# Kernel optimization log

Hardware: AMD Instinct MI355X
Metric: run time of the kernel (lower is better)

The kernel has to match this reference:

```python
import jax, jax.numpy as jnp
import numpy as np

K = 7  # local_kernel_size


def conv2d(x, w, b, pad):
    # x: [B,C,H,W], w: [O,I,kh,kw]
    y = jax.lax.conv_general_dilated(
        x, w, window_strides=(1, 1), padding=[(pad, pad), (pad, pad)],
        dimension_numbers=("NCHW", "OIHW", "NCHW"))
    return y + b[None, :, None, None]


def kernel_normalize(kernel, k):
    # kernel: [B, k*k, H, W]; zero-mean over tap dim, then add 1/(k*k)
    km = jnp.mean(kernel, axis=1, keepdims=True)
    return kernel - km + 1.0 / (k * k)


def local_conv_feat(img, kernel, k):
    # Fused dynamic local conv: avoids materializing [B,C,k*k,H,W].
    # Tap order matches F.unfold row-major (dy, dx).
    B, C, H, W = img.shape
    pad = (k - 1) // 2
    imgp = jnp.pad(img, ((0, 0), (0, 0), (pad, pad), (pad, pad)))
    out = jnp.zeros_like(img)
    for dy in range(k):
        for dx in range(k):
            idx = dy * k + dx
            out = out + imgp[:, :, dy:dy + H, dx:dx + W] * kernel[:, idx:idx + 1]
    return out


def setup_inputs() -> dict:
    key = jax.random.key(0)
    ks = jax.random.split(key, 14)
    B, C, H, W = 4, 64, 128, 128
    w = lambda k, shape: jax.random.normal(k, shape, jnp.float32) * 0.05
    return {
        "x": jax.random.normal(ks[0], (B, C, H, W), jnp.float32),
        "kernel_features": jax.random.normal(ks[1], (B, C, H, W), jnp.float32),
        # feature_path: two 3x3 convs
        "fw1": w(ks[2], (C, C, 3, 3)), "fb1": jnp.zeros((C,), jnp.float32),
        "fw2": w(ks[3], (C, C, 3, 3)), "fb2": jnp.zeros((C,), jnp.float32),
        # multiplicative_path: two 3x3 convs
        "mw1": w(ks[4], (C, C, 3, 3)), "mb1": jnp.zeros((C,), jnp.float32),
        "mw2": w(ks[5], (C, C, 3, 3)), "mb2": jnp.zeros((C,), jnp.float32),
        # local_filter_path: two 1x1 convs, last outputs k*k channels
        "lw1": w(ks[6], (C, C, 1, 1)), "lb1": jnp.zeros((C,), jnp.float32),
        "lw2": w(ks[7], (K * K, C, 1, 1)), "lb2": jnp.zeros((K * K,), jnp.float32),
    }


def reference(x, kernel_features, fw1, fb1, fw2, fb2, mw1, mb1, mw2, mb2, lw1, lb1, lw2, lb2):
    # feature_path: ReLU -> conv3x3 -> ReLU -> conv3x3
    fp = conv2d(jax.nn.relu(conv2d(jax.nn.relu(x), fw1, fb1, 1)), fw2, fb2, 1)
    # multiplicative_path: conv3x3 -> ReLU -> conv3x3
    mp = conv2d(jax.nn.relu(conv2d(kernel_features, mw1, mb1, 1)), mw2, mb2, 1)
    # local_filter_path: conv1x1 -> ReLU -> conv1x1 (-> k*k channels)
    lp = conv2d(jax.nn.relu(conv2d(kernel_features, lw1, lb1, 0)), lw2, lb2, 0)
    lp = kernel_normalize(lp, K)
    feat = fp * mp
    filtered = local_conv_feat(feat, lp, K)
    return x + filtered
```

## Files before the change

kernel.cpp:

```cpp
#include <hip/hip_runtime.h>
#include <hip/hip_bf16.h>

#define Cc 64
#define Hc 128
#define Wc 128
#define HWc (Hc * Wc)
#define Bc 4

typedef __attribute__((ext_vector_type(8))) short short8;
typedef __attribute__((ext_vector_type(4))) float float4v;

static __device__ __forceinline__ unsigned short f2bu(float f) {
    __hip_bfloat16 h = __float2bfloat16(f);
    return *(unsigned short*)&h;
}
static __device__ __forceinline__ float bulo(unsigned int u) {
    return __uint_as_float((u & 0xffffu) << 16);
}
static __device__ __forceinline__ float buhi(unsigned int u) {
    return __uint_as_float(u & 0xffff0000u);
}

static __device__ __forceinline__ void gl_lds16(const void* g, void* l) {
    __builtin_amdgcn_global_load_lds(
        (const __attribute__((address_space(1))) unsigned int*)g,
        (__attribute__((address_space(3))) unsigned int*)l, 16, 0, 0);
}

__global__ __launch_bounds__(256) void prep_k(
    const float* __restrict__ x, const float* __restrict__ kf,
    const float* __restrict__ fw1, const float* __restrict__ fw2,
    const float* __restrict__ mw1, const float* __restrict__ mw2,
    const float* __restrict__ lw1, const float* __restrict__ lw2,
    unsigned short* __restrict__ xb, unsigned short* __restrict__ kfb,
    unsigned short* __restrict__ wbase, unsigned short* __restrict__ zpage)
{
    const int bid = blockIdx.x;
    const int tid = threadIdx.x;

    if (bid < 512) {
        const bool isx = bid < 256;
        const float* src = isx ? x : kf;
        unsigned short* dst = isx ? xb : kfb;
        const int px = (isx ? bid : bid - 256) * 256 + tid;
        const int b  = px >> 14;
        const int hw = px & 16383;
        const float* s = src + (size_t)b * Cc * HWc + hw;
        unsigned short* d = dst + (size_t)px * Cc;
#pragma unroll
        for (int c8 = 0; c8 < 8; ++c8) {
            unsigned int pk[4];
#pragma unroll
            for (int jp = 0; jp < 4; ++jp) {
                float v0 = s[(size_t)(c8 * 8 + jp * 2 + 0) * HWc];
                float v1 = s[(size_t)(c8 * 8 + jp * 2 + 1) * HWc];
                if (isx) { v0 = fmaxf(v0, 0.f); v1 = fmaxf(v1, 0.f); }
                pk[jp] = (unsigned int)f2bu(v0) | ((unsigned int)f2bu(v1) << 16);
            }
            *(uint4*)(d + c8 * 8) = make_uint4(pk[0], pk[1], pk[2], pk[3]);
        }
    } else if (bid < 584) {
        const int wbid  = bid - 512;
        const int which = wbid / 18;
        const float* w = (which == 0) ? fw1 : (which == 1) ? fw2 : (which == 2) ? mw1 : mw2;
        unsigned short* wb = wbase + (size_t)which * 36864;
        const int g = (wbid % 18) * 256 + tid;
        if (g >= 4608) return;
        const int lane = g & 63;
        const int smt  = g >> 6;
        const int s    = smt >> 2;
        const int mt   = smt & 3;
        const int co   = mt * 16 + (lane & 15);
        const int kb   = s * 32 + (lane >> 4) * 8;
        unsigned int pk[4];
#pragma unroll
        for (int jp = 0; jp < 4; ++jp) {
            int k0 = kb + jp * 2, k1 = k0 + 1;
            float v0 = w[((size_t)co * Cc + (k0 & 63)) * 9 + (k0 >> 6)];
            float v1 = w[((size_t)co * Cc + (k1 & 63)) * 9 + (k1 >> 6)];
            pk[jp] = (unsigned int)f2bu(v0) | ((unsigned int)f2bu(v1) << 16);
        }
        *(uint4*)(wb + (size_t)g * 8) = make_uint4(pk[0], pk[1], pk[2], pk[3]);
    } else if (bid < 588) {
        const int wbid  = bid - 584;
        const int which = wbid >> 1;
        const float* w = which ? lw2 : lw1;
        const int Cout = which ? 49 : 64;
        unsigned short* wb = wbase + 4 * 36864 + (size_t)which * 4096;
        const int g = (wbid & 1) * 256 + tid;
        const int lane = g & 63;
        const int smt  = g >> 6;
        const int s    = smt >> 2;
        const int mt   = smt & 3;
        const int co   = mt * 16 + (lane & 15);
        const int kb   = s * 32 + (lane >> 4) * 8;
        unsigned int pk[4];
#pragma unroll
        for (int jp = 0; jp < 4; ++jp) {
            int k0 = kb + jp * 2, k1 = k0 + 1;
            float v0 = (co < Cout) ? w[(size_t)co * Cc + k0] : 0.f;
            float v1 = (co < Cout) ? w[(size_t)co * Cc + k1] : 0.f;
            pk[jp] = (unsigned int)f2bu(v0) | ((unsigned int)f2bu(v1) << 16);
        }
        *(uint4*)(wb + (size_t)g * 8) = make_uint4(pk[0], pk[1], pk[2], pk[3]);
    } else {
        if (tid < 64) ((unsigned int*)zpage)[tid] = 0;
    }
}

#define STAGE_DMA(INPTR, SBUF)                                                \
    for (int k = wv; k < 33; k += 4) {                                        \
        const int u_  = k * 8 + (lane >> 3);                                  \
        const int j_  = lane & 7;                                             \
        const int r_  = u_ / 66;                                              \
        const int c_  = u_ - r_ * 66;                                         \
        const int gh_ = h0 - 1 + r_;                                          \
        const int gw_ = w0 - 1 + c_;                                          \
        const bool ok_ = ((unsigned)gh_ < (unsigned)Hc) && ((unsigned)gw_ < (unsigned)Wc); \
        const int ch_ = j_ ^ (u_ & 7);                                        \
        const unsigned short* g_ = ok_                                        \
            ? (INPTR) + ((((size_t)b * Hc + gh_) * Wc + gw_) << 6) + (ch_ << 3) \
            : zpage + (ch_ << 3);                                             \
        gl_lds16(g_, &(SBUF)[k * 512]);                                       \
    }

#define LOAD_A(W, s, m) (*(const short8*)((W) + (size_t)(s) * 2048 + (size_t)(m) * 512))
#define LOAD_B(SB, s, nt) ({                                                  \
        const int tap_ = (s) >> 1;                                            \
        const int qb_  = rowb[tap_ / 3] + tap_ % 3;                           \
        const int ch0_ = ((s) & 1) * 4 + quad;                                \
        *(const short8*)&(SB)[(qb_ + (nt) * 16) * 64 + ((ch0_ ^ (qb_ & 7)) << 3)]; })

#define CONV_GEMM(APTR, ACC, SB)                                              \
    {                                                                         \
        short8 a_buf[4][2], b_cur[4], b_nxt[4];                               \
        _Pragma("unroll")                                                     \
        for (int q = 0; q < 3; ++q)                                           \
            _Pragma("unroll")                                                 \
            for (int m = 0; m < 2; ++m) a_buf[q][m] = LOAD_A(APTR, q, m);     \
        _Pragma("unroll")                                                     \
        for (int nt = 0; nt < 4; ++nt) b_cur[nt] = LOAD_B(SB, 0, nt);         \
        _Pragma("unroll")                                                     \
        for (int s = 0; s < 18; ++s) {                                        \
            if (s + 3 < 18) {                                                 \
                _Pragma("unroll")                                             \
                for (int m = 0; m < 2; ++m)                                   \
                    a_buf[(s + 3) & 3][m] = LOAD_A(APTR, s + 3, m);           \
            }                                                                 \
            if (s + 1 < 18) {                                                 \
                _Pragma("unroll")                                             \
                for (int nt = 0; nt < 4; ++nt)                                \
                    b_nxt[nt] = LOAD_B(SB, s + 1, nt);                        \
            }                                                                 \
            _Pragma("unroll")                                                 \
            for (int nt = 0; nt < 4; ++nt)                                    \
                _Pragma("unroll")                                             \
                for (int m = 0; m < 2; ++m)                                   \
                    ACC[m][nt] = __builtin_amdgcn_mfma_f32_16x16x32_bf16(     \
                        a_buf[s & 3][m], b_cur[nt], ACC[m][nt], 0, 0, 0);     \
            if (s + 1 < 18) {                                                 \
                _Pragma("unroll")                                             \
                for (int nt = 0; nt < 4; ++nt) b_cur[nt] = b_nxt[nt];         \
            }                                                                 \
        }                                                                     \
    }

__global__ __launch_bounds__(256) void conv1_lp_k(
    const unsigned short* __restrict__ in0,
    const unsigned short* __restrict__ in1,
    const unsigned short* __restrict__ wfrag0,
    const unsigned short* __restrict__ wfrag1,
    const float* __restrict__ bias0,
    const float* __restrict__ bias1,
    const unsigned short* __restrict__ zpage,
    unsigned short* __restrict__ out0,
    unsigned short* __restrict__ out1,
    const unsigned short* __restrict__ w1, const float* __restrict__ b1,
    const unsigned short* __restrict__ w2, const float* __restrict__ b2,
    unsigned short* __restrict__ lpout)
{
    __shared__ unsigned short s_b[264 * 64];

    const int tid  = threadIdx.x;
    const int lane = tid & 63;
    const int wv   = tid >> 6;
    const int quad = lane >> 4;
    const int glin = blockIdx.x;
    const int xcd  = glin & 7;
    const int slot = glin >> 3;

    if (slot < 128) {
        const int sel = slot >> 6;
        const int hti = slot & 63;
        const int b   = xcd >> 1;
        const int w0  = (xcd & 1) * 64;
        const int h0  = hti * 2;

        const unsigned short* in    = sel ? in1 : in0;
        const unsigned short* wfrag = sel ? wfrag1 : wfrag0;
        const float*          bias  = sel ? bias1 : bias0;
        unsigned short*       out   = sel ? out1 : out0;

        STAGE_DMA(in, s_b);
        __syncthreads();

        const int rowsel = wv >> 1;
        const int cohalf = wv & 1;
        const int n15    = lane & 15;
        const unsigned short* aptr = wfrag + (((size_t)(cohalf * 2) * 64 + lane) << 3);

        int rowb[3];
#pragma unroll
        for (int ky = 0; ky < 3; ++ky) rowb[ky] = (rowsel + ky) * 66 + n15;

        float4v acc[2][4];
#pragma unroll
        for (int m = 0; m < 2; ++m)
#pragma unroll
            for (int nt = 0; nt < 4; ++nt) acc[m][nt] = (float4v){0.f, 0.f, 0.f, 0.f};

        CONV_GEMM(aptr, acc, s_b);

        const int h = h0 + rowsel;
#pragma unroll
        for (int m = 0; m < 2; ++m) {
            const int mt  = cohalf * 2 + m;
            const int co0 = mt * 16 + quad * 4;
            float4 bv = *(const float4*)&bias[co0];
#pragma unroll
            for (int nt = 0; nt < 4; ++nt) {
                const size_t pix = ((size_t)b * Hc + h) * Wc + w0 + nt * 16 + n15;
                ushort4 pk;
                pk.x = f2bu(fmaxf(acc[m][nt][0] + bv.x, 0.f));
                pk.y = f2bu(fmaxf(acc[m][nt][1] + bv.y, 0.f));
                pk.z = f2bu(fmaxf(acc[m][nt][2] + bv.z, 0.f));
                pk.w = f2bu(fmaxf(acc[m][nt][3] + bv.w, 0.f));
                *(ushort4*)&out[pix * Cc + co0] = pk;
            }
        }
    } else {
        const int lpid = xcd * 128 + (slot - 128);
        const int p    = lane & 15;
        const size_t pix = (size_t)lpid * 64 + wv * 16 + p;
        unsigned short* st = &s_b[wv * 1024];

        float4v acc1[4];
#pragma unroll
        for (int mt = 0; mt < 4; ++mt) acc1[mt] = (float4v){0.f, 0.f, 0.f, 0.f};
#pragma unroll
        for (int s = 0; s < 2; ++s) {
            short8 bfr = *(const short8*)&in1[pix * Cc + s * 32 + quad * 8];
#pragma unroll
            for (int mt = 0; mt < 4; ++mt) {
                short8 afr = *(const short8*)&w1[(size_t)(((s * 4 + mt) << 6) + lane) << 3];
                acc1[mt] = __builtin_amdgcn_mfma_f32_16x16x32_bf16(afr, bfr, acc1[mt], 0, 0, 0);
            }
        }

#pragma unroll
        for (int mt = 0; mt < 4; ++mt) {
            const int co0 = mt * 16 + quad * 4;
            float4 bv = *(const float4*)&b1[co0];
            ushort4 pk;
            pk.x = f2bu(fmaxf(acc1[mt][0] + bv.x, 0.f));
            pk.y = f2bu(fmaxf(acc1[mt][1] + bv.y, 0.f));
            pk.z = f2bu(fmaxf(acc1[mt][2] + bv.z, 0.f));
            pk.w = f2bu(fmaxf(acc1[mt][3] + bv.w, 0.f));
            const int cg = co0 >> 3;
            *(ushort4*)&st[p * 64 + ((cg ^ (p & 7)) << 3) + (quad & 1) * 4] = pk;
        }
        __syncthreads();

        float4v acc2[4];
#pragma unroll
        for (int mt = 0; mt < 4; ++mt) acc2[mt] = (float4v){0.f, 0.f, 0.f, 0.f};
#pragma unroll
        for (int s = 0; s < 2; ++s) {
            const int cg = s * 4 + quad;
            short8 bfr = *(const short8*)&st[p * 64 + ((cg ^ (p & 7)) << 3)];
#pragma unroll
            for (int mt = 0; mt < 4; ++mt) {
                short8 afr = *(const short8*)&w2[(size_t)(((s * 4 + mt) << 6) + lane) << 3];
                acc2[mt] = __builtin_amdgcn_mfma_f32_16x16x32_bf16(afr, bfr, acc2[mt], 0, 0, 0);
            }
        }

        float v[4][4];
        float partial = 0.f;
#pragma unroll
        for (int mt = 0; mt < 4; ++mt) {
#pragma unroll
            for (int r = 0; r < 4; ++r) {
                const int tap = mt * 16 + quad * 4 + r;
                float val = (tap < 49) ? (acc2[mt][r] + b2[tap]) : 0.f;
                v[mt][r] = val;
                partial += val;
            }
        }
        partial += __shfl_xor(partial, 16, 64);
        partial += __shfl_xor(partial, 32, 64);
        const float m = partial * (1.f / 49.f) - (1.f / 49.f);

        const int b  = (int)(pix >> 14);
        const int hw = (int)(pix & 16383);
#pragma unroll
        for (int mt = 0; mt < 4; ++mt) {
#pragma unroll
            for (int r = 0; r < 4; ++r) {
                const int tap = mt * 16 + quad * 4 + r;
                if (tap < 49)
                    lpout[((size_t)b * 49 + tap) * HWc + hw] = f2bu(v[mt][r] - m);
            }
        }
    }
}

__global__ __launch_bounds__(256) void conv2_fused_k(
    const unsigned short* __restrict__ t1f,
    const unsigned short* __restrict__ t1m,
    const unsigned short* __restrict__ wf,
    const unsigned short* __restrict__ wm,
    const float* __restrict__ bf,
    const float* __restrict__ bm,
    const unsigned short* __restrict__ zpage,
    unsigned short* __restrict__ featp)
{
    __shared__ unsigned short s_b2[2][264 * 64];

    const int tid  = threadIdx.x;
    const int lane = tid & 63;
    const int wv   = tid >> 6;
    const int glin = blockIdx.x;
    const int xcd  = glin & 7;
    const int slot = glin >> 3;
    const int b    = xcd >> 1;
    const int w0   = (xcd & 1) * 64;
    const int h0   = slot * 2;

    STAGE_DMA(t1f, s_b2[0]);
    STAGE_DMA(t1m, s_b2[1]);
    __syncthreads();

    const int rowsel = wv >> 1;
    const int cohalf = wv & 1;
    const int quad   = lane >> 4;
    const int n15    = lane & 15;

    int rowb[3];
#pragma unroll
    for (int ky = 0; ky < 3; ++ky) rowb[ky] = (rowsel + ky) * 66 + n15;

    float4v acc[2][4];
#pragma unroll
    for (int m = 0; m < 2; ++m)
#pragma unroll
        for (int nt = 0; nt < 4; ++nt) acc[m][nt] = (float4v){0.f, 0.f, 0.f, 0.f};

    {
        const unsigned short* aptr = wf + (((size_t)(cohalf * 2) * 64 + lane) << 3);
        CONV_GEMM(aptr, acc, s_b2[0]);
    }

    float fpv[2][4][4];
#pragma unroll
    for (int m = 0; m < 2; ++m) {
        const int mt  = cohalf * 2 + m;
        const int co0 = mt * 16 + quad * 4;
        float4 bv = *(const float4*)&bf[co0];
#pragma unroll
        for (int nt = 0; nt < 4; ++nt) {
            fpv[m][nt][0] = bulo((unsigned int)f2bu(acc[m][nt][0] + bv.x));
            fpv[m][nt][1] = bulo((unsigned int)f2bu(acc[m][nt][1] + bv.y));
            fpv[m][nt][2] = bulo((unsigned int)f2bu(acc[m][nt][2] + bv.z));
            fpv[m][nt][3] = bulo((unsigned int)f2bu(acc[m][nt][3] + bv.w));
        }
    }

#pragma unroll
    for (int m = 0; m < 2; ++m)
#pragma unroll
        for (int nt = 0; nt < 4; ++nt) acc[m][nt] = (float4v){0.f, 0.f, 0.f, 0.f};

    {
        const unsigned short* aptr = wm + (((size_t)(cohalf * 2) * 64 + lane) << 3);
        CONV_GEMM(aptr, acc, s_b2[1]);
    }

    const int h = h0 + rowsel;
#pragma unroll
    for (int m = 0; m < 2; ++m) {
        const int mt  = cohalf * 2 + m;
        const int co0 = mt * 16 + quad * 4;
        float4 bv = *(const float4*)&bm[co0];
#pragma unroll
        for (int nt = 0; nt < 4; ++nt) {
            const int px = h * Wc + w0 + nt * 16 + n15;
            float v[4] = {acc[m][nt][0] + bv.x, acc[m][nt][1] + bv.y,
                          acc[m][nt][2] + bv.z, acc[m][nt][3] + bv.w};
#pragma unroll
            for (int r = 0; r < 4; ++r)
                featp[((size_t)b * Cc + co0 + r) * HWc + px] =
                    f2bu(v[r] * fpv[m][nt][r]);
        }
    }
}

__global__ __launch_bounds__(256) void local_conv_v4(
    const float* __restrict__ x, const unsigned short* __restrict__ featp,
    const unsigned short* __restrict__ lp, float* __restrict__ out)
{
    const int tid  = threadIdx.x;
    const int glin = blockIdx.x;
    const int xcd  = glin & 7;
    const int slot = glin >> 3;
    const int pair = xcd * 8 + (slot >> 4);
    const int cg   = slot & 15;
    const int b    = pair >> 4;
    const int hti  = pair & 15;

    const int w4  = (tid & 31) * 4;
    const int ro  = tid >> 5;
    const int h   = hti * 8 + ro;
    const int c0  = cg * 4;

    float msk[12];
#pragma unroll
    for (int e = 0; e < 12; ++e) {
        int gw = w4 - 4 + e;
        msk[e] = ((unsigned)gw < (unsigned)Wc) ? 1.f : 0.f;
    }

    float acc[4][4];
#pragma unroll
    for (int ch = 0; ch < 4; ++ch)
#pragma unroll
        for (int p = 0; p < 4; ++p) acc[ch][p] = 0.f;

    const unsigned short* lpb = lp + (size_t)b * 49 * HWc + (size_t)h * Wc + w4;
    const unsigned short* fb  = featp + ((size_t)b * Cc + c0) * HWc;

#pragma unroll
    for (int dy = 0; dy < 7; ++dy) {
        const int gh = h + dy - 3;
        if ((unsigned)gh >= (unsigned)Hc) continue;

        float lpf[7][4];
#pragma unroll
        for (int dx = 0; dx < 7; ++dx) {
            uint2 lv = *(const uint2*)&lpb[(size_t)(dy * 7 + dx) * HWc];
            lpf[dx][0] = bulo(lv.x); lpf[dx][1] = buhi(lv.x);
            lpf[dx][2] = bulo(lv.y); lpf[dx][3] = buhi(lv.y);
        }

        const unsigned short* frow = fb + (size_t)gh * Wc + w4;
#pragma unroll
        for (int ch = 0; ch < 4; ++ch) {
            const unsigned short* fr = frow + (size_t)ch * HWc;
            uint2 a  = *(const uint2*)(fr - 4);
            uint2 bq = *(const uint2*)(fr);
            uint2 cq = *(const uint2*)(fr + 4);
            float f[12];
            f[0]  = bulo(a.x);             f[1]  = buhi(a.x) * msk[1];
            f[2]  = bulo(a.y) * msk[2];    f[3]  = buhi(a.y) * msk[3];
            f[4]  = bulo(bq.x);            f[5]  = buhi(bq.x);
            f[6]  = bulo(bq.y);            f[7]  = buhi(bq.y);
            f[8]  = bulo(cq.x) * msk[8];   f[9]  = buhi(cq.x) * msk[9];
            f[10] = bulo(cq.y) * msk[10];  f[11] = buhi(cq.y);
#pragma unroll
            for (int dx = 0; dx < 7; ++dx)
#pragma unroll
                for (int p = 0; p < 4; ++p)
                    acc[ch][p] = fmaf(f[p + dx + 1], lpf[dx][p], acc[ch][p]);
        }
    }

#pragma unroll
    for (int ch = 0; ch < 4; ++ch) {
        const size_t idx = ((size_t)b * Cc + c0 + ch) * HWc + (size_t)h * Wc + w4;
        float4 xv = *(const float4*)&x[idx];
        float4 r  = {acc[ch][0] + xv.x, acc[ch][1] + xv.y,
                     acc[ch][2] + xv.z, acc[ch][3] + xv.w};
        *(float4*)&out[idx] = r;
    }
}

extern "C" void kernel_launch(void* const* d_in, const int* in_sizes, int n_in,
                              void* d_out, int out_size, void* d_ws, size_t ws_size,
                              hipStream_t stream)
{
    const float* x   = (const float*)d_in[0];
    const float* kf  = (const float*)d_in[1];
    const float* fw1 = (const float*)d_in[2];
    const float* fb1 = (const float*)d_in[3];
    const float* fw2 = (const float*)d_in[4];
    const float* fb2 = (const float*)d_in[5];
    const float* mw1 = (const float*)d_in[6];
    const float* mb1 = (const float*)d_in[7];
    const float* mw2 = (const float*)d_in[8];
    const float* mb2 = (const float*)d_in[9];
    const float* lw1 = (const float*)d_in[10];
    const float* lb1 = (const float*)d_in[11];
    const float* lw2 = (const float*)d_in[12];
    const float* lb2 = (const float*)d_in[13];

    float* out = (float*)d_out;
    char*  ws  = (char*)d_ws;

    const size_t NBH = (size_t)Bc * HWc * Cc * 2;
    const size_t LPH = (size_t)Bc * 49 * HWc * 2;
    const size_t WBA = (size_t)(4 * 36864 + 2 * 4096) * 2;

    unsigned short* t1f   = (unsigned short*)(ws);
    unsigned short* t1m   = (unsigned short*)(ws + NBH);
    unsigned short* featp = (unsigned short*)(ws + 2 * NBH);
    unsigned short* lpb   = (unsigned short*)(ws + 3 * NBH);
    unsigned short* xb    = (unsigned short*)(ws + 3 * NBH + LPH);
    unsigned short* kfb   = (unsigned short*)((char*)xb + NBH);
    unsigned short* wbase = (unsigned short*)((char*)kfb + NBH);
    unsigned short* zpage = (unsigned short*)((char*)wbase + WBA);
    unsigned short* wb1   = wbase;
    unsigned short* wb2   = wbase + 36864;
    unsigned short* wb3   = wbase + 2 * 36864;
    unsigned short* wb4   = wbase + 3 * 36864;
    unsigned short* wl1   = wbase + 4 * 36864;
    unsigned short* wl2   = wbase + 4 * 36864 + 4096;

    dim3 blk(256);

    prep_k<<<dim3(589), blk, 0, stream>>>(x, kf, fw1, fw2, mw1, mw2, lw1, lw2,
                                          xb, kfb, wbase, zpage);

    conv1_lp_k<<<dim3(2048), blk, 0, stream>>>(xb, kfb, wb1, wb3, fb1, mb1, zpage,
                                               t1f, t1m, wl1, lb1, wl2, lb2, lpb);

    conv2_fused_k<<<dim3(512), blk, 0, stream>>>(t1f, t1m, wb2, wb4, fb2, mb2,
                                                 zpage, featp);

    local_conv_v4<<<dim3(1024), blk, 0, stream>>>(x, featp, lpb, out);
}
```

Before: 161.6 us.

## Fuse local-filter 1x1 path into kf conv blocks and vectorize prep transpose

The separate local-filter-path blocks in conv1_lp_k are removed. Each block that convolves kernel_features now also computes the two 1x1 convs and the tap normalization for the pixels it just staged, which halves the grid. The prep kernel's NCHW to NHWC bf16 conversion now uses float4 loads, with each thread handling four pixels, so fewer blocks are needed. The zero page is also enlarged. The fusion adds imbalance, since only half the conv blocks carry the extra 1x1 work, and it lengthens the per-block critical path.

```diff
diff --git a/kernel.cpp b/kernel.cpp
--- a/kernel.cpp
+++ b/kernel.cpp
@@ -19,6 +19,9 @@
 }
 static __device__ __forceinline__ float buhi(unsigned int u) {
     return __uint_as_float(u & 0xffff0000u);
+}
+static __device__ __forceinline__ unsigned int pk2(float a, float b) {
+    return (unsigned int)f2bu(a) | ((unsigned int)f2bu(b) << 16);
 }
 
 static __device__ __forceinline__ void gl_lds16(const void* g, void* l) {
@@ -38,29 +41,40 @@
     const int bid = blockIdx.x;
     const int tid = threadIdx.x;
 
-    if (bid < 512) {
-        const bool isx = bid < 256;
-        const float* src = isx ? x : kf;
-        unsigned short* dst = isx ? xb : kfb;
-        const int px = (isx ? bid : bid - 256) * 256 + tid;
-        const int b  = px >> 14;
-        const int hw = px & 16383;
-        const float* s = src + (size_t)b * Cc * HWc + hw;
-        unsigned short* d = dst + (size_t)px * Cc;
-#pragma unroll
-        for (int c8 = 0; c8 < 8; ++c8) {
-            unsigned int pk[4];
+    if (bid < 256) {
+        const int gid    = bid * 256 + tid;
+        const int tensor = gid >> 15;
+        const int b      = (gid >> 13) & 3;
+        const int chalf  = (gid >> 12) & 1;
+        const int px     = (gid & 4095) * 4;
+        const bool isx   = (tensor == 0);
+        const float* s = (isx ? x : kf) + ((size_t)(b * Cc + chalf * 32)) * HWc + px;
+        unsigned short* d = (isx ? xb : kfb) + ((size_t)((size_t)b * HWc + px)) * Cc + chalf * 32;
+#pragma unroll
+        for (int c8 = 0; c8 < 4; ++c8) {
+            unsigned int pk[4][4];
 #pragma unroll
             for (int jp = 0; jp < 4; ++jp) {
-                float v0 = s[(size_t)(c8 * 8 + jp * 2 + 0) * HWc];
-                float v1 = s[(size_t)(c8 * 8 + jp * 2 + 1) * HWc];
-                if (isx) { v0 = fmaxf(v0, 0.f); v1 = fmaxf(v1, 0.f); }
-                pk[jp] = (unsigned int)f2bu(v0) | ((unsigned int)f2bu(v1) << 16);
+                float4 v0 = *(const float4*)(s + (size_t)(c8 * 8 + jp * 2 + 0) * HWc);
+                float4 v1 = *(const float4*)(s + (size_t)(c8 * 8 + jp * 2 + 1) * HWc);
+                if (isx) {
+                    v0.x = fmaxf(v0.x, 0.f); v0.y = fmaxf(v0.y, 0.f);
+                    v0.z = fmaxf(v0.z, 0.f); v0.w = fmaxf(v0.w, 0.f);
+                    v1.x = fmaxf(v1.x, 0.f); v1.y = fmaxf(v1.y, 0.f);
+                    v1.z = fmaxf(v1.z, 0.f); v1.w = fmaxf(v1.w, 0.f);
+                }
+                pk[0][jp] = pk2(v0.x, v1.x);
+                pk[1][jp] = pk2(v0.y, v1.y);
+                pk[2][jp] = pk2(v0.z, v1.z);
+                pk[3][jp] = pk2(v0.w, v1.w);
             }
-            *(uint4*)(d + c8 * 8) = make_uint4(pk[0], pk[1], pk[2], pk[3]);
-        }
-    } else if (bid < 584) {
-        const int wbid  = bid - 512;
+#pragma unroll
+            for (int i = 0; i < 4; ++i)
+                *(uint4*)(d + (size_t)i * Cc + c8 * 8) =
+                    make_uint4(pk[i][0], pk[i][1], pk[i][2], pk[i][3]);
+        }
+    } else if (bid < 328) {
+        const int wbid  = bid - 256;
         const int which = wbid / 18;
         const float* w = (which == 0) ? fw1 : (which == 1) ? fw2 : (which == 2) ? mw1 : mw2;
         unsigned short* wb = wbase + (size_t)which * 36864;
@@ -78,11 +92,11 @@
             int k0 = kb + jp * 2, k1 = k0 + 1;
             float v0 = w[((size_t)co * Cc + (k0 & 63)) * 9 + (k0 >> 6)];
             float v1 = w[((size_t)co * Cc + (k1 & 63)) * 9 + (k1 >> 6)];
-            pk[jp] = (unsigned int)f2bu(v0) | ((unsigned int)f2bu(v1) << 16);
+            pk[jp] = pk2(v0, v1);
         }
         *(uint4*)(wb + (size_t)g * 8) = make_uint4(pk[0], pk[1], pk[2], pk[3]);
-    } else if (bid < 588) {
-        const int wbid  = bid - 584;
+    } else if (bid < 332) {
+        const int wbid  = bid - 328;
         const int which = wbid >> 1;
         const float* w = which ? lw2 : lw1;
         const int Cout = which ? 49 : 64;
@@ -100,11 +114,13 @@
             int k0 = kb + jp * 2, k1 = k0 + 1;
             float v0 = (co < Cout) ? w[(size_t)co * Cc + k0] : 0.f;
             float v1 = (co < Cout) ? w[(size_t)co * Cc + k1] : 0.f;
-            pk[jp] = (unsigned int)f2bu(v0) | ((unsigned int)f2bu(v1) << 16);
+            pk[jp] = pk2(v0, v1);
         }
         *(uint4*)(wb + (size_t)g * 8) = make_uint4(pk[0], pk[1], pk[2], pk[3]);
     } else {
-        if (tid < 64) ((unsigned int*)zpage)[tid] = 0;
+        uint4 z = make_uint4(0u, 0u, 0u, 0u);
+        ((uint4*)zpage)[tid] = z;
+        ((uint4*)zpage)[256 + tid] = z;
     }
 }
 
@@ -189,127 +205,132 @@
     const int xcd  = glin & 7;
     const int slot = glin >> 3;
 
-    if (slot < 128) {
-        const int sel = slot >> 6;
-        const int hti = slot & 63;
-        const int b   = xcd >> 1;
-        const int w0  = (xcd & 1) * 64;
-        const int h0  = hti * 2;
-
-        const unsigned short* in    = sel ? in1 : in0;
-        const unsigned short* wfrag = sel ? wfrag1 : wfrag0;
-        const float*          bias  = sel ? bias1 : bias0;
-        unsigned short*       out   = sel ? out1 : out0;
-
-        STAGE_DMA(in, s_b);
+    const int sel = slot >> 6;
+    const int hti = slot & 63;
+    const int b   = xcd >> 1;
+    const int w0  = (xcd & 1) * 64;
+    const int h0  = hti * 2;
+
+    const unsigned short* in    = sel ? in1 : in0;
+    const unsigned short* wfrag = sel ? wfrag1 : wfrag0;
+    const float*          bias  = sel ? bias1 : bias0;
+    unsigned short*       out   = sel ? out1 : out0;
+
+    STAGE_DMA(in, s_b);
+    __syncthreads();
+
+    const int rowsel = wv >> 1;
+    const int cohalf = wv & 1;
+    const int n15    = lane & 15;
+    const unsigned short* aptr = wfrag + (((size_t)(cohalf * 2) * 64 + lane) << 3);
+
+    int rowb[3];
+#pragma unroll
+    for (int ky = 0; ky < 3; ++ky) rowb[ky] = (rowsel + ky) * 66 + n15;
+
+    float4v acc[2][4];
+#pragma unroll
+    for (int m = 0; m < 2; ++m)
+#pragma unroll
+        for (int nt = 0; nt < 4; ++nt) acc[m][nt] = (float4v){0.f, 0.f, 0.f, 0.f};
+
+    CONV_GEMM(aptr, acc, s_b);
+
+    const int h = h0 + rowsel;
+#pragma unroll
+    for (int m = 0; m < 2; ++m) {
+        const int mt  = cohalf * 2 + m;
+        const int co0 = mt * 16 + quad * 4;
+        float4 bv = *(const float4*)&bias[co0];
+#pragma unroll
+        for (int nt = 0; nt < 4; ++nt) {
+            const size_t pix = ((size_t)b * Hc + h) * Wc + w0 + nt * 16 + n15;
+            ushort4 pk;
+            pk.x = f2bu(fmaxf(acc[m][nt][0] + bv.x, 0.f));
+            pk.y = f2bu(fmaxf(acc[m][nt][1] + bv.y, 0.f));
+            pk.z = f2bu(fmaxf(acc[m][nt][2] + bv.z, 0.f));
+            pk.w = f2bu(fmaxf(acc[m][nt][3] + bv.w, 0.f));
+            *(ushort4*)&out[pix * Cc + co0] = pk;
+        }
+    }
+
+    if (sel == 1) {
         __syncthreads();
 
-        const int rowsel = wv >> 1;
-        const int cohalf = wv & 1;
-        const int n15    = lane & 15;
-        const unsigned short* aptr = wfrag + (((size_t)(cohalf * 2) * 64 + lane) << 3);
-
-        int rowb[3];
-#pragma unroll
-        for (int ky = 0; ky < 3; ++ky) rowb[ky] = (rowsel + ky) * 66 + n15;
-
-        float4v acc[2][4];
-#pragma unroll
-        for (int m = 0; m < 2; ++m)
-#pragma unroll
-            for (int nt = 0; nt < 4; ++nt) acc[m][nt] = (float4v){0.f, 0.f, 0.f, 0.f};
-
-        CONV_GEMM(aptr, acc, s_b);
-
-        const int h = h0 + rowsel;
-#pragma unroll
-        for (int m = 0; m < 2; ++m) {
-            const int mt  = cohalf * 2 + m;
-            const int co0 = mt * 16 + quad * 4;
-            float4 bv = *(const float4*)&bias[co0];
-#pragma unroll
-            for (int nt = 0; nt < 4; ++nt) {
-                const size_t pix = ((size_t)b * Hc + h) * Wc + w0 + nt * 16 + n15;
+        const int p = lane & 15;
+#pragma unroll 1
+        for (int ui = 0; ui < 2; ++ui) {
+            const int hl = h0 + ui;
+            const size_t pix = ((size_t)b * Hc + hl) * Wc + w0 + wv * 16 + p;
+            unsigned short* st = &s_b[(size_t)(ui * 4 + wv) * 1024];
+
+            float4v acc1[4];
+#pragma unroll
+            for (int mt = 0; mt < 4; ++mt) acc1[mt] = (float4v){0.f, 0.f, 0.f, 0.f};
+#pragma unroll
+            for (int s = 0; s < 2; ++s) {
+                short8 bfr = *(const short8*)&in1[pix * Cc + s * 32 + quad * 8];
+#pragma unroll
+                for (int mt = 0; mt < 4; ++mt) {
+                    short8 afr = *(const short8*)&w1[(size_t)(((s * 4 + mt) << 6) + lane) << 3];
+                    acc1[mt] = __builtin_amdgcn_mfma_f32_16x16x32_bf16(afr, bfr, acc1[mt], 0, 0, 0);
+                }
+            }
+
+#pragma unroll
+            for (int mt = 0; mt < 4; ++mt) {
+                const int co0 = mt * 16 + quad * 4;
+                float4 bv = *(const float4*)&b1[co0];
                 ushort4 pk;
-                pk.x = f2bu(fmaxf(acc[m][nt][0] + bv.x, 0.f));
-                pk.y = f2bu(fmaxf(acc[m][nt][1] + bv.y, 0.f));
-                pk.z = f2bu(fmaxf(acc[m][nt][2] + bv.z, 0.f));
-                pk.w = f2bu(fmaxf(acc[m][nt][3] + bv.w, 0.f));
-                *(ushort4*)&out[pix * Cc + co0] = pk;
+                pk.x = f2bu(fmaxf(acc1[mt][0] + bv.x, 0.f));
+                pk.y = f2bu(fmaxf(acc1[mt][1] + bv.y, 0.f));
+                pk.z = f2bu(fmaxf(acc1[mt][2] + bv.z, 0.f));
+                pk.w = f2bu(fmaxf(acc1[mt][3] + bv.w, 0.f));
+                const int cg = co0 >> 3;
+                *(ushort4*)&st[p * 64 + ((cg ^ (p & 7)) << 3) + (quad & 1) * 4] = pk;
             }
-        }
-    } else {
-        const int lpid = xcd * 128 + (slot - 128);
-        const int p    = lane & 15;
-        const size_t pix = (size_t)lpid * 64 + wv * 16 + p;
-        unsigned short* st = &s_b[wv * 1024];
-
-        float4v acc1[4];
-#pragma unroll
-        for (int mt = 0; mt < 4; ++mt) acc1[mt] = (float4v){0.f, 0.f, 0.f, 0.f};
-#pragma unroll
-        for (int s = 0; s < 2; ++s) {
-            short8 bfr = *(const short8*)&in1[pix * Cc + s * 32 + quad * 8];
+            __syncthreads();
+
+            float4v acc2[4];
+#pragma unroll
+            for (int mt = 0; mt < 4; ++mt) acc2[mt] = (float4v){0.f, 0.f, 0.f, 0.f};
+#pragma unroll
+            for (int s = 0; s < 2; ++s) {
+                const int cg = s * 4 + quad;
+                short8 bfr = *(const short8*)&st[p * 64 + ((cg ^ (p & 7)) << 3)];
+#pragma unroll
+                for (int mt = 0; mt < 4; ++mt) {
+                    short8 afr = *(const short8*)&w2[(size_t)(((s * 4 + mt) << 6) + lane) << 3];
+                    acc2[mt] = __builtin_amdgcn_mfma_f32_16x16x32_bf16(afr, bfr, acc2[mt], 0, 0, 0);
+                }
+            }
+
+            float v[4][4];
+            float partial = 0.f;
 #pragma unroll
             for (int mt = 0; mt < 4; ++mt) {
-                short8 afr = *(const short8*)&w1[(size_t)(((s * 4 + mt) << 6) + lane) << 3];
-                acc1[mt] = __builtin_amdgcn_mfma_f32_16x16x32_bf16(afr, bfr, acc1[mt], 0, 0, 0);
+#pragma unroll
+                for (int r = 0; r < 4; ++r) {
+                    const int tap = mt * 16 + quad * 4 + r;
+                    float val = (tap < 49) ? (acc2[mt][r] + b2[tap]) : 0.f;
+                    v[mt][r] = val;
+                    partial += val;
+                }
             }
-        }
-
-#pragma unroll
-        for (int mt = 0; mt < 4; ++mt) {
-            const int co0 = mt * 16 + quad * 4;
-            float4 bv = *(const float4*)&b1[co0];
-            ushort4 pk;
-            pk.x = f2bu(fmaxf(acc1[mt][0] + bv.x, 0.f));
-            pk.y = f2bu(fmaxf(acc1[mt][1] + bv.y, 0.f));
-            pk.z = f2bu(fmaxf(acc1[mt][2] + bv.z, 0.f));
-            pk.w = f2bu(fmaxf(acc1[mt][3] + bv.w, 0.f));
-            const int cg = co0 >> 3;
-            *(ushort4*)&st[p * 64 + ((cg ^ (p & 7)) << 3) + (quad & 1) * 4] = pk;
-        }
-        __syncthreads();
-
-        float4v acc2[4];
-#pragma unroll
-        for (int mt = 0; mt < 4; ++mt) acc2[mt] = (float4v){0.f, 0.f, 0.f, 0.f};
-#pragma unroll
-        for (int s = 0; s < 2; ++s) {
-            const int cg = s * 4 + quad;
-            short8 bfr = *(const short8*)&st[p * 64 + ((cg ^ (p & 7)) << 3)];
+            partial += __shfl_xor(partial, 16, 64);
+            partial += __shfl_xor(partial, 32, 64);
+            const float m = partial * (1.f / 49.f) - (1.f / 49.f);
+
+            const int bI = (int)(pix >> 14);
+            const int hw = (int)(pix & 16383);
 #pragma unroll
             for (int mt = 0; mt < 4; ++mt) {
-                short8 afr = *(const short8*)&w2[(size_t)(((s * 4 + mt) << 6) + lane) << 3];
-                acc2[mt] = __builtin_amdgcn_mfma_f32_16x16x32_bf16(afr, bfr, acc2[mt], 0, 0, 0);
-            }
-        }
-
-        float v[4][4];
-        float partial = 0.f;
-#pragma unroll
-        for (int mt = 0; mt < 4; ++mt) {
-#pragma unroll
-            for (int r = 0; r < 4; ++r) {
-                const int tap = mt * 16 + quad * 4 + r;
-                float val = (tap < 49) ? (acc2[mt][r] + b2[tap]) : 0.f;
-                v[mt][r] = val;
-                partial += val;
-            }
-        }
-        partial += __shfl_xor(partial, 16, 64);
-        partial += __shfl_xor(partial, 32, 64);
-        const float m = partial * (1.f / 49.f) - (1.f / 49.f);
-
-        const int b  = (int)(pix >> 14);
-        const int hw = (int)(pix & 16383);
-#pragma unroll
-        for (int mt = 0; mt < 4; ++mt) {
-#pragma unroll
-            for (int r = 0; r < 4; ++r) {
-                const int tap = mt * 16 + quad * 4 + r;
-                if (tap < 49)
-                    lpout[((size_t)b * 49 + tap) * HWc + hw] = f2bu(v[mt][r] - m);
+#pragma unroll
+                for (int r = 0; r < 4; ++r) {
+                    const int tap = mt * 16 + quad * 4 + r;
+                    if (tap < 49)
+                        lpout[((size_t)bI * 49 + tap) * HWc + hw] = f2bu(v[mt][r] - m);
+                }
             }
         }
     }
@@ -527,10 +548,10 @@
 
     dim3 blk(256);
 
-    prep_k<<<dim3(589), blk, 0, stream>>>(x, kf, fw1, fw2, mw1, mw2, lw1, lw2,
+    prep_k<<<dim3(333), blk, 0, stream>>>(x, kf, fw1, fw2, mw1, mw2, lw1, lw2,
                                           xb, kfb, wbase, zpage);
 
-    conv1_lp_k<<<dim3(2048), blk, 0, stream>>>(xb, kfb, wb1, wb3, fb1, mb1, zpage,
+    conv1_lp_k<<<dim3(1024), blk, 0, stream>>>(xb, kfb, wb1, wb3, fb1, mb1, zpage,
                                                t1f, t1m, wl1, lb1, wl2, lb2, lpb);
 
     conv2_fused_k<<<dim3(512), blk, 0, stream>>>(t1f, t1m, wb2, wb4, fb2, mb2,
```

Result: slower. 169.5 us (+4.9%).
